# Kernel optimization log

Hardware: AMD Instinct MI355X
Metric: run time of the kernel (lower is better)

## Reference

```python
import jax, jax.numpy as jnp
import numpy as np

H, W = 496, 432  # ny, nx
C = 64           # pillar_dim == hidden_dim == NUM_BEV_FEATURES
B, N = 2, 8192   # batch size, non-empty pillars per batch
EPS = 1e-5


def _ln(x, g, b):
    m = jnp.mean(x, axis=-1, keepdims=True)
    v = jnp.var(x, axis=-1, keepdims=True)
    return (x - m) * jax.lax.rsqrt(v + EPS) * g + b


def _apply_rope(x):
    # x: [H, W, C] -> 2D RoPE-rotated features, matching torch reference math
    half = C // 2
    theta = 10000.0 ** (-(jnp.arange(half, dtype=jnp.float32) / half))
    h = jnp.linspace(-1.0, 1.0, H)
    w = jnp.linspace(-1.0, 1.0, W)
    hs = jnp.sin(h[:, None, None] * theta)  # [H,1,half]
    hc = jnp.cos(h[:, None, None] * theta)
    ws = jnp.sin(w[None, :, None] * theta)  # [1,W,half]
    wc = jnp.cos(w[None, :, None] * theta)
    x1, x2 = x[..., :half], x[..., half:]
    return jnp.concatenate(
        [x1 * hc * wc - x2 * hs * ws, x1 * hs * ws + x2 * hc * wc], axis=-1)


def setup_inputs() -> dict:
    key = jax.random.key(0)
    ks = jax.random.split(key, 8)
    rng = np.random.default_rng(0)
    # sorted UNIQUE flat indices per batch (boolean-mask gather order == sorted index order)
    idx = np.stack([np.sort(rng.choice(H * W, size=N, replace=False)) for _ in range(B)])
    s = 0.05
    return {
        "pillar_features": jax.random.normal(ks[0], (B, N, C), jnp.float32),
        "voxel_indices": jnp.asarray(idx, jnp.int32),
        "q_w": jax.random.normal(ks[1], (C, C), jnp.float32) * s,
        "q_b": jnp.zeros((C,), jnp.float32),
        "k_w": jax.random.normal(ks[2], (C, C), jnp.float32) * s,
        "k_b": jnp.zeros((C,), jnp.float32),
        "v_w": jax.random.normal(ks[3], (C, C), jnp.float32) * s,
        "v_b": jnp.zeros((C,), jnp.float32),
        "ffn_w1": jax.random.normal(ks[4], (C, C), jnp.float32) * s,
        "ffn_b1": jnp.zeros((C,), jnp.float32),
        "ffn_w2": jax.random.normal(ks[5], (C, C), jnp.float32) * s,
        "ffn_b2": jnp.zeros((C,), jnp.float32),
        "n1_g": jnp.ones((C,), jnp.float32),
        "n1_b": jnp.zeros((C,), jnp.float32),
        "n2_g": jnp.ones((C,), jnp.float32),
        "n2_b": jnp.zeros((C,), jnp.float32),
    }


def reference(pillar_features, voxel_indices, q_w, q_b, k_w, k_b, v_w, v_b,
              ffn_w1, ffn_b1, ffn_w2, ffn_b2, n1_g, n1_b, n2_g, n2_b):
    def per_batch(pillars, idx):
        # scatter pillars to dense BEV grid [H*W, C]
        dense = jnp.zeros((H * W, C), pillars.dtype).at[idx].set(pillars)
        x = dense.reshape(H, W, C)
        x = x + _apply_rope(x)                  # residual RoPE add
        flat = x.reshape(H * W, C)
        g = flat[idx]                           # masked gather (sorted index order)
        gn = _ln(g, n1_g, n1_b)
        Q = gn @ q_w.T + q_b                    # [N, C]
        K = gn @ k_w.T + k_b
        V = gn @ v_w.T + v_b
        attn = jax.nn.softmax(Q @ K.T, axis=-1)  # [N, N] full attention
        att = attn @ V + g
        h1 = jax.nn.gelu(_ln(att, n2_g, n2_b) @ ffn_w1.T + ffn_b1, approximate=False)
        upd = h1 @ ffn_w2.T + ffn_b2 + att
        out = flat.at[idx].set(upd)             # scatter back
        return out.T.reshape(C, H, W)
    return jax.vmap(per_batch)(pillar_features, voxel_indices)  # [B, C, H, W]
```

## Files before the change

kernel.cpp:

```cpp
#include <hip/hip_runtime.h>
#include <hip/hip_bf16.h>
#include <math.h>

#define HH 496
#define WW 432
#define CC 64
#define BB 2
#define NN 8192
#define HW_ (HH * WW)
#define SPLIT 8
#define KVPS (NN / SPLIT)
#define LOG2E 1.44269504088896f
#define DEFER_THR 11.541560327f

#if __has_builtin(__builtin_amdgcn_exp2f)
#define EXP2(x) __builtin_amdgcn_exp2f(x)
#else
#define EXP2(x) exp2f(x)
#endif

typedef __attribute__((ext_vector_type(8))) short bhalf8;
typedef __attribute__((ext_vector_type(4))) float f32x4;

__device__ __forceinline__ unsigned short f2bf(float f) {
  union { float f; unsigned int u; } v; v.f = f;
  unsigned int r = (v.u + 0x7fffu + ((v.u >> 16) & 1u)) >> 16;
  return (unsigned short)r;
}

__device__ __forceinline__ float bf2f(unsigned short u) {
  union { unsigned int u; float f; } v;
  v.u = ((unsigned int)u) << 16;
  return v.f;
}

__device__ __forceinline__ void gload16(const void* g, void* l) {
  __builtin_amdgcn_global_load_lds(
      (const __attribute__((address_space(1))) void*)g,
      (__attribute__((address_space(3))) void*)l, 16, 0, 0);
}

__global__ void prep_kernel(float* __restrict__ tabHS, float* __restrict__ tabHC,
                            float* __restrict__ tabWS, float* __restrict__ tabWC,
                            int* __restrict__ map) {
  int tid = blockIdx.x * blockDim.x + threadIdx.x;
  const int ntab = (HH + WW) * 32;
  if (tid < ntab) {
    int j = tid & 31;
    float theta = __expf(-(float)j * (9.210340371976184f / 32.f));
    if (tid < HH * 32) {
      int i = tid >> 5;
      float h = -1.f + 2.f * (float)i / (float)(HH - 1);
      float a = h * theta;
      tabHS[tid] = sinf(a);
      tabHC[tid] = cosf(a);
    } else {
      int t2 = tid - HH * 32;
      int i = t2 >> 5;
      float w = -1.f + 2.f * (float)i / (float)(WW - 1);
      float a = w * theta;
      tabWS[t2] = sinf(a);
      tabWC[t2] = cosf(a);
    }
  } else if (tid < ntab + BB * HW_) {
    map[tid - ntab] = -1;
  }
}

__global__ __launch_bounds__(256) void qkv_kernel(
    const float* __restrict__ pillar, const int* __restrict__ vidx,
    const float* __restrict__ tabHS, const float* __restrict__ tabHC,
    const float* __restrict__ tabWS, const float* __restrict__ tabWC,
    const float* __restrict__ qw, const float* __restrict__ kw,
    const float* __restrict__ vw,
    const float* __restrict__ qb, const float* __restrict__ kbias,
    const float* __restrict__ vb,
    const float* __restrict__ n1g, const float* __restrict__ n1b,
    float* __restrict__ g_out, unsigned short* __restrict__ Qb,
    unsigned short* __restrict__ Kb, unsigned short* __restrict__ Vt,
    int* __restrict__ map) {
  __shared__ unsigned short Aln[64][72];
  __shared__ unsigned short Wq[64][72], Wk[64][72], Wv[64][72];
  __shared__ unsigned int Vbo[64][36];
  int tid = threadIdx.x, wid = tid >> 6, lane = tid & 63;
  int l16 = lane & 15, lg = lane >> 4;
  int pt0 = blockIdx.x * 64;
  int b = pt0 >> 13, n0 = pt0 & (NN - 1);

  {
    int c = tid >> 2, k0 = (tid & 3) * 16;
#pragma unroll
    for (int mmm = 0; mmm < 3; mmm++) {
      const float* src = (mmm == 0 ? qw : mmm == 1 ? kw : vw) + c * 64 + k0;
      unsigned int pk[8];
#pragma unroll
      for (int j = 0; j < 8; j++) {
        float lo = src[2 * j], hi = src[2 * j + 1];
        asm("v_cvt_pk_bf16_f32 %0, %1, %2" : "=v"(pk[j]) : "v"(lo), "v"(hi));
      }
      unsigned short(*Wm)[72] = mmm == 0 ? Wq : mmm == 1 ? Wk : Wv;
      unsigned int* dst = (unsigned int*)&Wm[c][k0];
      *(uint4*)dst = make_uint4(pk[0], pk[1], pk[2], pk[3]);
      *(uint4*)(dst + 4) = make_uint4(pk[4], pk[5], pk[6], pk[7]);
    }
  }

  float n1g_l = n1g[lane], n1b_l = n1b[lane];
#pragma unroll 4
  for (int i = 0; i < 16; i++) {
    int p = wid * 16 + i;
    int pt = pt0 + p;
    float x = pillar[(size_t)pt * CC + lane];
    int pos = vidx[pt];
    int h = pos / WW, w = pos - h * WW;
    int j = lane & 31;
    float x1 = __shfl(x, j), x2 = __shfl(x, j + 32);
    float hs = tabHS[h * 32 + j], hc = tabHC[h * 32 + j];
    float ws = tabWS[w * 32 + j], wc = tabWC[w * 32 + j];
    float rope = (lane < 32) ? (x1 * hc * wc - x2 * hs * ws)
                             : (x1 * hs * ws + x2 * hc * wc);
    float gv = x + rope;
    g_out[(size_t)pt * CC + lane] = gv;
    float s = gv;
    for (int mm2 = 1; mm2 <= 32; mm2 <<= 1) s += __shfl_xor(s, mm2);
    float mean = s * (1.f / 64.f);
    float d = gv - mean;
    float vsum = d * d;
    for (int mm2 = 1; mm2 <= 32; mm2 <<= 1) vsum += __shfl_xor(vsum, mm2);
    float rstd = rsqrtf(vsum * (1.f / 64.f) + 1e-5f);
    float gn = d * rstd * n1g_l + n1b_l;
    Aln[p][lane] = f2bf(gn);
    if (lane == 0) map[b * HW_ + pos] = pt & (NN - 1);
  }
  __syncthreads();

  bhalf8 aG0 = *(bhalf8*)&Aln[wid * 16 + l16][lg * 8];
  bhalf8 aG1 = *(bhalf8*)&Aln[wid * 16 + l16][32 + lg * 8];
  float qb4[4], kb4[4], vb4[4];
#pragma unroll
  for (int ct = 0; ct < 4; ct++) {
    qb4[ct] = qb[ct * 16 + l16];
    kb4[ct] = kbias[ct * 16 + l16];
    vb4[ct] = vb[ct * 16 + l16];
  }
#pragma unroll
  for (int ct = 0; ct < 4; ct++) {
    bhalf8 bq0 = *(bhalf8*)&Wq[ct * 16 + l16][lg * 8];
    bhalf8 bq1 = *(bhalf8*)&Wq[ct * 16 + l16][32 + lg * 8];
    bhalf8 bk0 = *(bhalf8*)&Wk[ct * 16 + l16][lg * 8];
    bhalf8 bk1 = *(bhalf8*)&Wk[ct * 16 + l16][32 + lg * 8];
    bhalf8 bv0 = *(bhalf8*)&Wv[ct * 16 + l16][lg * 8];
    bhalf8 bv1 = *(bhalf8*)&Wv[ct * 16 + l16][32 + lg * 8];
    f32x4 dq = (f32x4){0.f, 0.f, 0.f, 0.f};
    f32x4 dk = (f32x4){0.f, 0.f, 0.f, 0.f};
    f32x4 dv = (f32x4){0.f, 0.f, 0.f, 0.f};
    dq = __builtin_amdgcn_mfma_f32_16x16x32_bf16(aG0, bq0, dq, 0, 0, 0);
    dq = __builtin_amdgcn_mfma_f32_16x16x32_bf16(aG1, bq1, dq, 0, 0, 0);
    dk = __builtin_amdgcn_mfma_f32_16x16x32_bf16(aG0, bk0, dk, 0, 0, 0);
    dk = __builtin_amdgcn_mfma_f32_16x16x32_bf16(aG1, bk1, dk, 0, 0, 0);
    dv = __builtin_amdgcn_mfma_f32_16x16x32_bf16(aG0, bv0, dv, 0, 0, 0);
    dv = __builtin_amdgcn_mfma_f32_16x16x32_bf16(aG1, bv1, dv, 0, 0, 0);
#pragma unroll
    for (int r = 0; r < 4; r++) {
      size_t gi = (size_t)(pt0 + wid * 16 + 4 * lg + r) * CC + ct * 16 + l16;
      Qb[gi] = f2bf((dq[r] + qb4[ct]) * LOG2E);
      Kb[gi] = f2bf(dk[r] + kb4[ct]);
    }
    float e0 = dv[0] + vb4[ct], e1 = dv[1] + vb4[ct];
    float e2 = dv[2] + vb4[ct], e3 = dv[3] + vb4[ct];
    unsigned int v0, v1;
    asm("v_cvt_pk_bf16_f32 %0, %1, %2" : "=v"(v0) : "v"(e0), "v"(e1));
    asm("v_cvt_pk_bf16_f32 %0, %1, %2" : "=v"(v1) : "v"(e2), "v"(e3));
    Vbo[ct * 16 + l16][wid * 8 + lg * 2 + 0] = v0;
    Vbo[ct * 16 + l16][wid * 8 + lg * 2 + 1] = v1;
  }
  __syncthreads();
  {
    int c = tid >> 2, ch = tid & 3;
    uint4 w0 = *(uint4*)&Vbo[c][ch * 8];
    uint4 w1 = *(uint4*)&Vbo[c][ch * 8 + 4];
    unsigned int* dst = (unsigned int*)(Vt + ((size_t)b * CC + c) * NN + n0 + ch * 16);
    *(uint4*)dst = w0;
    *(uint4*)(dst + 4) = w1;
  }
}

__global__ __attribute__((amdgpu_flat_work_group_size(512, 512),
                          amdgpu_waves_per_eu(4, 4))) void attn_kernel(
    const unsigned short* __restrict__ Qb, const unsigned short* __restrict__ Kb,
    const unsigned short* __restrict__ Vt,
    unsigned short* __restrict__ OPb, float* __restrict__ Mb,
    float* __restrict__ Lb) {
  __shared__ unsigned short Kt[2][64 * 64];
  __shared__ unsigned short Vl[2][64 * 64];
  __shared__ unsigned short Plds[8][32][72];
  int tidx = threadIdx.x;
  int wid = tidx >> 6, lane = tidx & 63;
  int l16 = lane & 15, lg = lane >> 4;
  int blk = blockIdx.x;
  int s = blk & (SPLIT - 1);
  int tb = blk >> 3;
  int b = tb >> 5;
  int tile = tb & 31;
  int q0 = tile * 256 + wid * 32;
  int kvbeg = s * KVPS;
  const unsigned short* Q = Qb + (size_t)b * NN * CC;
  const unsigned short* K = Kb + (size_t)b * NN * CC;
  const unsigned short* V = Vt + (size_t)b * CC * NN;

  bhalf8 bQ0 = *(const bhalf8*)(Q + (size_t)(q0 + l16) * CC + lg * 8);
  bhalf8 bQ1 = *(const bhalf8*)(Q + (size_t)(q0 + l16) * CC + 32 + lg * 8);
  bhalf8 bQ2 = *(const bhalf8*)(Q + (size_t)(q0 + 16 + l16) * CC + lg * 8);
  bhalf8 bQ3 = *(const bhalf8*)(Q + (size_t)(q0 + 16 + l16) * CC + 32 + lg * 8);

  int r8 = lane >> 3, chn = lane & 7;
  int sch = chn ^ r8;
  const unsigned short* Ksrc = K + (size_t)(8 * wid + r8) * CC + sch * 8;
  const unsigned short* Vsrc = V + (size_t)(8 * wid + r8) * NN + sch * 8;
  unsigned short* KtW = &Kt[0][0] + (8 * wid) * 64;
  unsigned short* VlW = &Vl[0][0] + (8 * wid) * 64;

  f32x4 acc0[4], acc1[4];
#pragma unroll
  for (int i = 0; i < 4; i++) {
    acc0[i] = (f32x4){0.f, 0.f, 0.f, 0.f};
    acc1[i] = (f32x4){0.f, 0.f, 0.f, 0.f};
  }
  float m = -1e30f, Lp0 = 0.f, Lp1 = 0.f;
  int sw8 = (l16 & 7) * 8;

  auto stage = [&](int bufi, int kv0) {
    gload16(Ksrc + (size_t)kv0 * CC, KtW + bufi * 4096);
    gload16(Vsrc + kv0, VlW + bufi * 4096);
  };

  auto body = [&](int buf, int kv0) {
    const unsigned short* Kb_ = &Kt[buf][0];
    const unsigned short* Vb_ = &Vl[buf][0];
    f32x4 St[4], Su[4];
    __builtin_amdgcn_s_setprio(1);
#pragma unroll
    for (int t = 0; t < 4; t++) {
      const unsigned short* kr = Kb_ + (16 * t + l16) * 64;
      bhalf8 aK0 = *(const bhalf8*)(kr + ((lg * 8) ^ sw8));
      bhalf8 aK1 = *(const bhalf8*)(kr + (((lg + 4) * 8) ^ sw8));
      f32x4 sa = (f32x4){0.f, 0.f, 0.f, 0.f};
      f32x4 sb = (f32x4){0.f, 0.f, 0.f, 0.f};
      sa = __builtin_amdgcn_mfma_f32_16x16x32_bf16(aK0, bQ0, sa, 0, 0, 0);
      sa = __builtin_amdgcn_mfma_f32_16x16x32_bf16(aK1, bQ1, sa, 0, 0, 0);
      sb = __builtin_amdgcn_mfma_f32_16x16x32_bf16(aK0, bQ2, sb, 0, 0, 0);
      sb = __builtin_amdgcn_mfma_f32_16x16x32_bf16(aK1, bQ3, sb, 0, 0, 0);
      St[t] = sa;
      Su[t] = sb;
    }
    __builtin_amdgcn_s_setprio(0);
    float m0a = fmaxf(fmaxf(St[0][0], St[0][1]), fmaxf(St[0][2], St[0][3]));
    float m0b = fmaxf(fmaxf(St[1][0], St[1][1]), fmaxf(St[1][2], St[1][3]));
    float m0c = fmaxf(fmaxf(St[2][0], St[2][1]), fmaxf(St[2][2], St[2][3]));
    float m0d = fmaxf(fmaxf(St[3][0], St[3][1]), fmaxf(St[3][2], St[3][3]));
    float m1a = fmaxf(fmaxf(Su[0][0], Su[0][1]), fmaxf(Su[0][2], Su[0][3]));
    float m1b = fmaxf(fmaxf(Su[1][0], Su[1][1]), fmaxf(Su[1][2], Su[1][3]));
    float m1c = fmaxf(fmaxf(Su[2][0], Su[2][1]), fmaxf(Su[2][2], Su[2][3]));
    float m1d = fmaxf(fmaxf(Su[3][0], Su[3][1]), fmaxf(Su[3][2], Su[3][3]));
    float pm = fmaxf(fmaxf(fmaxf(m0a, m0b), fmaxf(m0c, m0d)),
                     fmaxf(fmaxf(m1a, m1b), fmaxf(m1c, m1d)));
    pm = fmaxf(pm, __shfl_xor(pm, 16));
    pm = fmaxf(pm, __shfl_xor(pm, 32));
    if (!__all(pm <= m + DEFER_THR)) {
      float mn = fmaxf(m, pm);
      float sc = EXP2(m - mn);
      m = mn;
      float scq[4];
#pragma unroll
      for (int r = 0; r < 4; r++) scq[r] = __shfl(sc, 4 * lg + r);
#pragma unroll
      for (int cg = 0; cg < 4; cg++)
#pragma unroll
        for (int r = 0; r < 4; r++) {
          acc0[cg][r] *= scq[r];
          acc1[cg][r] *= scq[r];
        }
      Lp0 *= sc;
      Lp1 *= sc;
    }
#pragma unroll
    for (int t = 0; t < 4; t++)
#pragma unroll
      for (int r = 0; r < 4; r++) {
        float p0 = EXP2(St[t][r] - m);
        float p1 = EXP2(Su[t][r] - m);
        St[t][r] = p0; Su[t][r] = p1;
        Lp0 += p0; Lp1 += p1;
      }
#pragma unroll
    for (int t = 0; t < 4; t++) {
      unsigned int pw0, pw1, pw2, pw3;
      float a0 = St[t][0], a1 = St[t][1], a2 = St[t][2], a3 = St[t][3];
      float b0 = Su[t][0], b1 = Su[t][1], b2 = Su[t][2], b3 = Su[t][3];
      asm("v_cvt_pk_bf16_f32 %0, %1, %2" : "=v"(pw0) : "v"(a0), "v"(a1));
      asm("v_cvt_pk_bf16_f32 %0, %1, %2" : "=v"(pw1) : "v"(a2), "v"(a3));
      asm("v_cvt_pk_bf16_f32 %0, %1, %2" : "=v"(pw2) : "v"(b0), "v"(b1));
      asm("v_cvt_pk_bf16_f32 %0, %1, %2" : "=v"(pw3) : "v"(b2), "v"(b3));
      *(uint2*)&Plds[wid][l16][16 * t + 4 * lg] = make_uint2(pw0, pw1);
      *(uint2*)&Plds[wid][16 + l16][16 * t + 4 * lg] = make_uint2(pw2, pw3);
    }
#pragma unroll
    for (int ch = 0; ch < 2; ch++) {
      bhalf8 aP0 = *(bhalf8*)&Plds[wid][l16][ch * 32 + lg * 8];
      bhalf8 aP1 = *(bhalf8*)&Plds[wid][16 + l16][ch * 32 + lg * 8];
      __builtin_amdgcn_s_setprio(1);
#pragma unroll
      for (int cg = 0; cg < 4; cg++) {
        bhalf8 bV = *(const bhalf8*)(Vb_ + (cg * 16 + l16) * 64 +
                                     (((4 * ch + lg) * 8) ^ sw8));
        acc0[cg] = __builtin_amdgcn_mfma_f32_16x16x32_bf16(aP0, bV, acc0[cg], 0, 0, 0);
        acc1[cg] = __builtin_amdgcn_mfma_f32_16x16x32_bf16(aP1, bV, acc1[cg], 0, 0, 0);
      }
      __builtin_amdgcn_s_setprio(0);
    }
  };

  stage(0, kvbeg);
  __syncthreads();
  const int nstep = KVPS / 64;
  for (int stp = 0; stp < nstep; stp += 2) {
    int kv0 = kvbeg + stp * 64;
    if (stp + 1 < nstep) stage(1, kv0 + 64);
    body(0, kv0);
    __syncthreads();
    if (stp + 2 < nstep) stage(0, kv0 + 128);
    body(1, kv0 + 64);
    __syncthreads();
  }
  size_t rowb = ((size_t)s * BB + b) * NN;
#pragma unroll
  for (int cg = 0; cg < 4; cg++)
#pragma unroll
    for (int r = 0; r < 4; r++) {
      OPb[(rowb + q0 + 4 * lg + r) * CC + cg * 16 + l16] = f2bf(acc0[cg][r]);
      OPb[(rowb + q0 + 16 + 4 * lg + r) * CC + cg * 16 + l16] = f2bf(acc1[cg][r]);
    }
  Lp0 += __shfl_xor(Lp0, 16);
  Lp0 += __shfl_xor(Lp0, 32);
  Lp1 += __shfl_xor(Lp1, 16);
  Lp1 += __shfl_xor(Lp1, 32);
  if (lg == 0) {
    Mb[rowb + q0 + l16] = m;
    Lb[rowb + q0 + l16] = Lp0;
    Mb[rowb + q0 + 16 + l16] = m;
    Lb[rowb + q0 + 16 + l16] = Lp1;
  }
}

__global__ __launch_bounds__(256) void ffn_kernel(
    const unsigned short* __restrict__ OPb, const float* __restrict__ Mb,
    const float* __restrict__ Lb, const float* __restrict__ g_in,
    const float* __restrict__ w1, const float* __restrict__ w2,
    const float* __restrict__ b1, const float* __restrict__ b2,
    const float* __restrict__ n2g, const float* __restrict__ n2b,
    float* __restrict__ upd) {
  __shared__ unsigned short Atile[64][72];
  __shared__ unsigned short Htile[64][72];
  __shared__ float aT[64][66];
  __shared__ unsigned short W1[64][72], W2[64][72];
  int tid = threadIdx.x, wid = tid >> 6, lane = tid & 63;
  int l16 = lane & 15, lg = lane >> 4;
  int pt0 = blockIdx.x * 64;

  {
    int c = tid >> 2, k0 = (tid & 3) * 16;
#pragma unroll
    for (int mmm = 0; mmm < 2; mmm++) {
      const float* src = (mmm == 0 ? w1 : w2) + c * 64 + k0;
      unsigned int pk[8];
#pragma unroll
      for (int j = 0; j < 8; j++) {
        float lo = src[2 * j], hi = src[2 * j + 1];
        asm("v_cvt_pk_bf16_f32 %0, %1, %2" : "=v"(pk[j]) : "v"(lo), "v"(hi));
      }
      unsigned short(*Wm)[72] = mmm == 0 ? W1 : W2;
      unsigned int* dst = (unsigned int*)&Wm[c][k0];
      *(uint4*)dst = make_uint4(pk[0], pk[1], pk[2], pk[3]);
      *(uint4*)(dst + 4) = make_uint4(pk[4], pk[5], pk[6], pk[7]);
    }
  }

  float n2g_l = n2g[lane], n2b_l = n2b[lane];
#pragma unroll 2
  for (int i = 0; i < 16; i++) {
    int p = wid * 16 + i;
    int pt = pt0 + p;
    float mv[SPLIT];
    float M = -1e30f;
#pragma unroll
    for (int s = 0; s < SPLIT; s++) {
      mv[s] = Mb[s * (BB * NN) + pt];
      M = fmaxf(M, mv[s]);
    }
    float accv = 0.f, Ls = 0.f;
#pragma unroll
    for (int s = 0; s < SPLIT; s++) {
      float w = EXP2(mv[s] - M);
      accv += w * bf2f(OPb[((size_t)s * (BB * NN) + pt) * CC + lane]);
      Ls += w * Lb[s * (BB * NN) + pt];
    }
    float a = accv / Ls + g_in[(size_t)pt * CC + lane];
    aT[p][lane] = a;
    float s2 = a;
    for (int mm2 = 1; mm2 <= 32; mm2 <<= 1) s2 += __shfl_xor(s2, mm2);
    float mean = s2 * (1.f / 64.f);
    float d = a - mean;
    float vsum = d * d;
    for (int mm2 = 1; mm2 <= 32; mm2 <<= 1) vsum += __shfl_xor(vsum, mm2);
    float rstd = rsqrtf(vsum * (1.f / 64.f) + 1e-5f);
    Atile[p][lane] = f2bf(d * rstd * n2g_l + n2b_l);
  }
  __syncthreads();

  bhalf8 aH0 = *(bhalf8*)&Atile[wid * 16 + l16][lg * 8];
  bhalf8 aH1 = *(bhalf8*)&Atile[wid * 16 + l16][32 + lg * 8];
  float b1v[4], b2v[4];
#pragma unroll
  for (int ct = 0; ct < 4; ct++) {
    b1v[ct] = b1[ct * 16 + l16];
    b2v[ct] = b2[ct * 16 + l16];
  }
#pragma unroll
  for (int ct = 0; ct < 4; ct++) {
    bhalf8 bw0 = *(bhalf8*)&W1[ct * 16 + l16][lg * 8];
    bhalf8 bw1 = *(bhalf8*)&W1[ct * 16 + l16][32 + lg * 8];
    f32x4 d1 = (f32x4){0.f, 0.f, 0.f, 0.f};
    d1 = __builtin_amdgcn_mfma_f32_16x16x32_bf16(aH0, bw0, d1, 0, 0, 0);
    d1 = __builtin_amdgcn_mfma_f32_16x16x32_bf16(aH1, bw1, d1, 0, 0, 0);
#pragma unroll
    for (int r = 0; r < 4; r++) {
      float h = d1[r] + b1v[ct];
      h = 0.5f * h * (1.f + erff(h * 0.70710678118654752f));
      Htile[wid * 16 + 4 * lg + r][ct * 16 + l16] = f2bf(h);
    }
  }
  __syncthreads();

  bhalf8 aF0 = *(bhalf8*)&Htile[wid * 16 + l16][lg * 8];
  bhalf8 aF1 = *(bhalf8*)&Htile[wid * 16 + l16][32 + lg * 8];
#pragma unroll
  for (int ct = 0; ct < 4; ct++) {
    bhalf8 bw0 = *(bhalf8*)&W2[ct * 16 + l16][lg * 8];
    bhalf8 bw1 = *(bhalf8*)&W2[ct * 16 + l16][32 + lg * 8];
    f32x4 d2 = (f32x4){0.f, 0.f, 0.f, 0.f};
    d2 = __builtin_amdgcn_mfma_f32_16x16x32_bf16(aF0, bw0, d2, 0, 0, 0);
    d2 = __builtin_amdgcn_mfma_f32_16x16x32_bf16(aF1, bw1, d2, 0, 0, 0);
#pragma unroll
    for (int r = 0; r < 4; r++) {
      int p = wid * 16 + 4 * lg + r;
      upd[(size_t)(pt0 + p) * CC + ct * 16 + l16] = d2[r] + b2v[ct] + aT[p][ct * 16 + l16];
    }
  }
}

__global__ __launch_bounds__(256) void out_kernel(
    const int* __restrict__ map, const float* __restrict__ upd,
    float* __restrict__ out) {
  int b = blockIdx.x / (HW_ / 256);
  int pos = (blockIdx.x % (HW_ / 256)) * 256 + threadIdx.x;
  int r = map[b * HW_ + pos];
  float4 vals[16];
  if (r >= 0) {
    const float4* up = (const float4*)(upd + ((size_t)b * NN + r) * CC);
#pragma unroll
    for (int i = 0; i < 16; i++) vals[i] = up[i];
  } else {
#pragma unroll
    for (int i = 0; i < 16; i++) vals[i] = make_float4(0.f, 0.f, 0.f, 0.f);
  }
  float* o = out + (size_t)b * CC * HW_ + pos;
#pragma unroll
  for (int i = 0; i < 16; i++) {
    o[(size_t)(4 * i + 0) * HW_] = vals[i].x;
    o[(size_t)(4 * i + 1) * HW_] = vals[i].y;
    o[(size_t)(4 * i + 2) * HW_] = vals[i].z;
    o[(size_t)(4 * i + 3) * HW_] = vals[i].w;
  }
}

extern "C" void kernel_launch(void* const* d_in, const int* in_sizes, int n_in,
                              void* d_out, int out_size, void* d_ws, size_t ws_size,
                              hipStream_t stream) {
  const float* pillar = (const float*)d_in[0];
  const int* vidx = (const int*)d_in[1];
  const float* qw = (const float*)d_in[2];
  const float* qb = (const float*)d_in[3];
  const float* kw = (const float*)d_in[4];
  const float* kb = (const float*)d_in[5];
  const float* vw = (const float*)d_in[6];
  const float* vb = (const float*)d_in[7];
  const float* w1 = (const float*)d_in[8];
  const float* b1 = (const float*)d_in[9];
  const float* w2 = (const float*)d_in[10];
  const float* b2 = (const float*)d_in[11];
  const float* n1g = (const float*)d_in[12];
  const float* n1b = (const float*)d_in[13];
  const float* n2g = (const float*)d_in[14];
  const float* n2b = (const float*)d_in[15];
  float* out = (float*)d_out;

  char* ws = (char*)d_ws;
  size_t off = 0;
  auto take = [&](size_t bytes) -> char* {
    off = (off + 255) & ~(size_t)255;
    char* p = ws + off;
    off += bytes;
    return p;
  };
  float* tabHS = (float*)take((size_t)HH * 32 * 4);
  float* tabHC = (float*)take((size_t)HH * 32 * 4);
  float* tabWS = (float*)take((size_t)WW * 32 * 4);
  float* tabWC = (float*)take((size_t)WW * 32 * 4);
  float* gbuf = (float*)take((size_t)BB * NN * CC * 4);
  float* updb = (float*)take((size_t)BB * NN * CC * 4);
  unsigned short* Qb = (unsigned short*)take((size_t)BB * NN * CC * 2);
  unsigned short* Kb = (unsigned short*)take((size_t)BB * NN * CC * 2);
  unsigned short* Vt = (unsigned short*)take((size_t)BB * CC * NN * 2);
  unsigned short* OPb = (unsigned short*)take((size_t)SPLIT * BB * NN * CC * 2);
  float* Mbuf = (float*)take((size_t)SPLIT * BB * NN * 4);
  float* Lbuf = (float*)take((size_t)SPLIT * BB * NN * 4);
  int* map = (int*)take((size_t)BB * HW_ * 4);

  int preptot = (HH + WW) * 32 + BB * HW_;
  prep_kernel<<<(preptot + 255) / 256, 256, 0, stream>>>(
      tabHS, tabHC, tabWS, tabWC, map);
  qkv_kernel<<<BB * NN / 64, 256, 0, stream>>>(
      pillar, vidx, tabHS, tabHC, tabWS, tabWC, qw, kw, vw, qb, kb, vb,
      n1g, n1b, gbuf, Qb, Kb, Vt, map);
  attn_kernel<<<BB * (NN / 256) * SPLIT, 512, 0, stream>>>(Qb, Kb, Vt, OPb, Mbuf, Lbuf);
  ffn_kernel<<<BB * NN / 64, 256, 0, stream>>>(OPb, Mbuf, Lbuf, gbuf, w1, w2,
                                               b1, b2, n2g, n2b, updb);
  out_kernel<<<BB * (HW_ / 256), 256, 0, stream>>>(map, updb, out);
}
```

Measured before the change: 108.5 us.

## Halve per-wave query rows in attention kernel and double block count

Each wave in the attention kernel now handles 16 query rows instead of 32, so a block covers 128 queries and the grid doubles. This halves accumulators and Q registers per wave and shrinks the P staging buffer. The launch bounds change from a fixed 4 waves per EU to allowing 6 blocks per CU, aiming for higher occupancy. The trade-off is that every K/V tile loaded into LDS is now reused by half as many queries, so K/V global and LDS traffic per query doubles.

```diff
diff --git a/kernel.cpp b/kernel.cpp
--- a/kernel.cpp
+++ b/kernel.cpp
@@ -185,24 +185,23 @@
   }
 }
 
-__global__ __attribute__((amdgpu_flat_work_group_size(512, 512),
-                          amdgpu_waves_per_eu(4, 4))) void attn_kernel(
+__global__ __launch_bounds__(512, 6) void attn_kernel(
     const unsigned short* __restrict__ Qb, const unsigned short* __restrict__ Kb,
     const unsigned short* __restrict__ Vt,
     unsigned short* __restrict__ OPb, float* __restrict__ Mb,
     float* __restrict__ Lb) {
   __shared__ unsigned short Kt[2][64 * 64];
   __shared__ unsigned short Vl[2][64 * 64];
-  __shared__ unsigned short Plds[8][32][72];
+  __shared__ unsigned short Plds[8][16][72];
   int tidx = threadIdx.x;
   int wid = tidx >> 6, lane = tidx & 63;
   int l16 = lane & 15, lg = lane >> 4;
   int blk = blockIdx.x;
   int s = blk & (SPLIT - 1);
   int tb = blk >> 3;
-  int b = tb >> 5;
-  int tile = tb & 31;
-  int q0 = tile * 256 + wid * 32;
+  int b = tb >> 6;
+  int tile = tb & 63;
+  int q0 = tile * 128 + wid * 16;
   int kvbeg = s * KVPS;
   const unsigned short* Q = Qb + (size_t)b * NN * CC;
   const unsigned short* K = Kb + (size_t)b * NN * CC;
@@ -210,8 +209,6 @@
 
   bhalf8 bQ0 = *(const bhalf8*)(Q + (size_t)(q0 + l16) * CC + lg * 8);
   bhalf8 bQ1 = *(const bhalf8*)(Q + (size_t)(q0 + l16) * CC + 32 + lg * 8);
-  bhalf8 bQ2 = *(const bhalf8*)(Q + (size_t)(q0 + 16 + l16) * CC + lg * 8);
-  bhalf8 bQ3 = *(const bhalf8*)(Q + (size_t)(q0 + 16 + l16) * CC + 32 + lg * 8);
 
   int r8 = lane >> 3, chn = lane & 7;
   int sch = chn ^ r8;
@@ -220,13 +217,10 @@
   unsigned short* KtW = &Kt[0][0] + (8 * wid) * 64;
   unsigned short* VlW = &Vl[0][0] + (8 * wid) * 64;
 
-  f32x4 acc0[4], acc1[4];
-#pragma unroll
-  for (int i = 0; i < 4; i++) {
-    acc0[i] = (f32x4){0.f, 0.f, 0.f, 0.f};
-    acc1[i] = (f32x4){0.f, 0.f, 0.f, 0.f};
-  }
-  float m = -1e30f, Lp0 = 0.f, Lp1 = 0.f;
+  f32x4 acc0[4];
+#pragma unroll
+  for (int i = 0; i < 4; i++) acc0[i] = (f32x4){0.f, 0.f, 0.f, 0.f};
+  float m = -1e30f, Lp0 = 0.f;
   int sw8 = (l16 & 7) * 8;
 
   auto stage = [&](int bufi, int kv0) {
@@ -237,7 +231,7 @@
   auto body = [&](int buf, int kv0) {
     const unsigned short* Kb_ = &Kt[buf][0];
     const unsigned short* Vb_ = &Vl[buf][0];
-    f32x4 St[4], Su[4];
+    f32x4 St[4];
     __builtin_amdgcn_s_setprio(1);
 #pragma unroll
     for (int t = 0; t < 4; t++) {
@@ -245,25 +239,16 @@
       bhalf8 aK0 = *(const bhalf8*)(kr + ((lg * 8) ^ sw8));
       bhalf8 aK1 = *(const bhalf8*)(kr + (((lg + 4) * 8) ^ sw8));
       f32x4 sa = (f32x4){0.f, 0.f, 0.f, 0.f};
-      f32x4 sb = (f32x4){0.f, 0.f, 0.f, 0.f};
       sa = __builtin_amdgcn_mfma_f32_16x16x32_bf16(aK0, bQ0, sa, 0, 0, 0);
       sa = __builtin_amdgcn_mfma_f32_16x16x32_bf16(aK1, bQ1, sa, 0, 0, 0);
-      sb = __builtin_amdgcn_mfma_f32_16x16x32_bf16(aK0, bQ2, sb, 0, 0, 0);
-      sb = __builtin_amdgcn_mfma_f32_16x16x32_bf16(aK1, bQ3, sb, 0, 0, 0);
       St[t] = sa;
-      Su[t] = sb;
     }
     __builtin_amdgcn_s_setprio(0);
-    float m0a = fmaxf(fmaxf(St[0][0], St[0][1]), fmaxf(St[0][2], St[0][3]));
-    float m0b = fmaxf(fmaxf(St[1][0], St[1][1]), fmaxf(St[1][2], St[1][3]));
-    float m0c = fmaxf(fmaxf(St[2][0], St[2][1]), fmaxf(St[2][2], St[2][3]));
-    float m0d = fmaxf(fmaxf(St[3][0], St[3][1]), fmaxf(St[3][2], St[3][3]));
-    float m1a = fmaxf(fmaxf(Su[0][0], Su[0][1]), fmaxf(Su[0][2], Su[0][3]));
-    float m1b = fmaxf(fmaxf(Su[1][0], Su[1][1]), fmaxf(Su[1][2], Su[1][3]));
-    float m1c = fmaxf(fmaxf(Su[2][0], Su[2][1]), fmaxf(Su[2][2], Su[2][3]));
-    float m1d = fmaxf(fmaxf(Su[3][0], Su[3][1]), fmaxf(Su[3][2], Su[3][3]));
-    float pm = fmaxf(fmaxf(fmaxf(m0a, m0b), fmaxf(m0c, m0d)),
-                     fmaxf(fmaxf(m1a, m1b), fmaxf(m1c, m1d)));
+    float ma = fmaxf(fmaxf(St[0][0], St[0][1]), fmaxf(St[0][2], St[0][3]));
+    float mb = fmaxf(fmaxf(St[1][0], St[1][1]), fmaxf(St[1][2], St[1][3]));
+    float mc = fmaxf(fmaxf(St[2][0], St[2][1]), fmaxf(St[2][2], St[2][3]));
+    float md = fmaxf(fmaxf(St[3][0], St[3][1]), fmaxf(St[3][2], St[3][3]));
+    float pm = fmaxf(fmaxf(ma, mb), fmaxf(mc, md));
     pm = fmaxf(pm, __shfl_xor(pm, 16));
     pm = fmaxf(pm, __shfl_xor(pm, 32));
     if (!__all(pm <= m + DEFER_THR)) {
@@ -276,45 +261,34 @@
 #pragma unroll
       for (int cg = 0; cg < 4; cg++)
 #pragma unroll
-        for (int r = 0; r < 4; r++) {
-          acc0[cg][r] *= scq[r];
-          acc1[cg][r] *= scq[r];
-        }
+        for (int r = 0; r < 4; r++) acc0[cg][r] *= scq[r];
       Lp0 *= sc;
-      Lp1 *= sc;
     }
 #pragma unroll
     for (int t = 0; t < 4; t++)
 #pragma unroll
       for (int r = 0; r < 4; r++) {
         float p0 = EXP2(St[t][r] - m);
-        float p1 = EXP2(Su[t][r] - m);
-        St[t][r] = p0; Su[t][r] = p1;
-        Lp0 += p0; Lp1 += p1;
+        St[t][r] = p0;
+        Lp0 += p0;
       }
 #pragma unroll
     for (int t = 0; t < 4; t++) {
-      unsigned int pw0, pw1, pw2, pw3;
+      unsigned int pw0, pw1;
       float a0 = St[t][0], a1 = St[t][1], a2 = St[t][2], a3 = St[t][3];
-      float b0 = Su[t][0], b1 = Su[t][1], b2 = Su[t][2], b3 = Su[t][3];
       asm("v_cvt_pk_bf16_f32 %0, %1, %2" : "=v"(pw0) : "v"(a0), "v"(a1));
       asm("v_cvt_pk_bf16_f32 %0, %1, %2" : "=v"(pw1) : "v"(a2), "v"(a3));
-      asm("v_cvt_pk_bf16_f32 %0, %1, %2" : "=v"(pw2) : "v"(b0), "v"(b1));
-      asm("v_cvt_pk_bf16_f32 %0, %1, %2" : "=v"(pw3) : "v"(b2), "v"(b3));
       *(uint2*)&Plds[wid][l16][16 * t + 4 * lg] = make_uint2(pw0, pw1);
-      *(uint2*)&Plds[wid][16 + l16][16 * t + 4 * lg] = make_uint2(pw2, pw3);
     }
 #pragma unroll
     for (int ch = 0; ch < 2; ch++) {
       bhalf8 aP0 = *(bhalf8*)&Plds[wid][l16][ch * 32 + lg * 8];
-      bhalf8 aP1 = *(bhalf8*)&Plds[wid][16 + l16][ch * 32 + lg * 8];
       __builtin_amdgcn_s_setprio(1);
 #pragma unroll
       for (int cg = 0; cg < 4; cg++) {
         bhalf8 bV = *(const bhalf8*)(Vb_ + (cg * 16 + l16) * 64 +
                                      (((4 * ch + lg) * 8) ^ sw8));
         acc0[cg] = __builtin_amdgcn_mfma_f32_16x16x32_bf16(aP0, bV, acc0[cg], 0, 0, 0);
-        acc1[cg] = __builtin_amdgcn_mfma_f32_16x16x32_bf16(aP1, bV, acc1[cg], 0, 0, 0);
       }
       __builtin_amdgcn_s_setprio(0);
     }
@@ -336,19 +310,13 @@
 #pragma unroll
   for (int cg = 0; cg < 4; cg++)
 #pragma unroll
-    for (int r = 0; r < 4; r++) {
+    for (int r = 0; r < 4; r++)
       OPb[(rowb + q0 + 4 * lg + r) * CC + cg * 16 + l16] = f2bf(acc0[cg][r]);
-      OPb[(rowb + q0 + 16 + 4 * lg + r) * CC + cg * 16 + l16] = f2bf(acc1[cg][r]);
-    }
   Lp0 += __shfl_xor(Lp0, 16);
   Lp0 += __shfl_xor(Lp0, 32);
-  Lp1 += __shfl_xor(Lp1, 16);
-  Lp1 += __shfl_xor(Lp1, 32);
   if (lg == 0) {
     Mb[rowb + q0 + l16] = m;
     Lb[rowb + q0 + l16] = Lp0;
-    Mb[rowb + q0 + 16 + l16] = m;
-    Lb[rowb + q0 + 16 + l16] = Lp1;
   }
 }
 
@@ -532,7 +500,7 @@
   qkv_kernel<<<BB * NN / 64, 256, 0, stream>>>(
       pillar, vidx, tabHS, tabHC, tabWS, tabWC, qw, kw, vw, qb, kb, vb,
       n1g, n1b, gbuf, Qb, Kb, Vt, map);
-  attn_kernel<<<BB * (NN / 256) * SPLIT, 512, 0, stream>>>(Qb, Kb, Vt, OPb, Mbuf, Lbuf);
+  attn_kernel<<<BB * (NN / 128) * SPLIT, 512, 0, stream>>>(Qb, Kb, Vt, OPb, Mbuf, Lbuf);
   ffn_kernel<<<BB * NN / 64, 256, 0, stream>>>(OPb, Mbuf, Lbuf, gbuf, w1, w2,
                                                b1, b2, n2g, n2b, updb);
   out_kernel<<<BB * (HW_ / 256), 256, 0, stream>>>(map, updb, out);
```

After: 113.3 us. 1.04x slower.
